# Performance work log

Measured on AMD Instinct MI355X. Metric: run time of the kernel, lower is better.

Reference implementation:

```python
import jax, jax.numpy as jnp
import numpy as np

D_MODEL = 3072
HEADS = 24
DH = 128
EPS = 1e-05


def _rmsnorm(x, w):
    # x: [..., DH], normalize over last dim in fp32
    var = jnp.mean(jnp.square(x.astype(jnp.float32)), axis=-1, keepdims=True)
    return (x * jax.lax.rsqrt(var + EPS)) * w


def _rope(x, cos, sin):
    # x: [B, S, H, D]; cos/sin: [S, D//2] (real/imag of complex freqs)
    xr = x[..., 0::2].astype(jnp.float32)
    xi = x[..., 1::2].astype(jnp.float32)
    c = cos[None, :, None, :]
    s = sin[None, :, None, :]
    out_r = xr * c - xi * s
    out_i = xr * s + xi * c
    out = jnp.stack([out_r, out_i], axis=-1)  # [B,S,H,D/2,2]
    return out.reshape(*x.shape).astype(x.dtype)


def _linear(x, w, b):
    # torch Linear convention: w [out, in]
    return jnp.einsum('bsi,oi->bso', x, w) + b


def setup_inputs() -> dict:
    key = jax.random.key(0)
    ks = jax.random.split(key, 24)
    B, S_IMG, S_TXT = 1, 2048, 256
    init = lambda k, shp: jax.random.normal(k, shp, dtype=jnp.float32) * 0.02
    inp = {
        'hidden_states': jax.random.normal(ks[0], (B, S_IMG, D_MODEL), dtype=jnp.float32),
        'encoder_hidden_states': jax.random.normal(ks[1], (B, S_TXT, D_MODEL), dtype=jnp.float32),
        'encoder_hidden_states_mask': jnp.ones((B, S_TXT), dtype=bool),
        'img_cos': jnp.cos(jax.random.uniform(ks[2], (S_IMG, DH // 2)) * 6.28),
        'img_sin': jnp.sin(jax.random.uniform(ks[2], (S_IMG, DH // 2)) * 6.28),
        'txt_cos': jnp.cos(jax.random.uniform(ks[3], (S_TXT, DH // 2)) * 6.28),
        'txt_sin': jnp.sin(jax.random.uniform(ks[3], (S_TXT, DH // 2)) * 6.28),
        'wq': init(ks[4], (D_MODEL, D_MODEL)), 'bq': jnp.zeros((D_MODEL,), jnp.float32),
        'wk': init(ks[5], (D_MODEL, D_MODEL)), 'bk': jnp.zeros((D_MODEL,), jnp.float32),
        'wv': init(ks[6], (D_MODEL, D_MODEL)), 'bv': jnp.zeros((D_MODEL,), jnp.float32),
        'awq': init(ks[7], (D_MODEL, D_MODEL)), 'abq': jnp.zeros((D_MODEL,), jnp.float32),
        'awk': init(ks[8], (D_MODEL, D_MODEL)), 'abk': jnp.zeros((D_MODEL,), jnp.float32),
        'awv': init(ks[9], (D_MODEL, D_MODEL)), 'abv': jnp.zeros((D_MODEL,), jnp.float32),
        'norm_q_w': jnp.ones((DH,), jnp.float32),
        'norm_k_w': jnp.ones((DH,), jnp.float32),
        'norm_aq_w': jnp.ones((DH,), jnp.float32),
        'norm_ak_w': jnp.ones((DH,), jnp.float32),
        'w_out': init(ks[10], (D_MODEL, D_MODEL)), 'b_out': jnp.zeros((D_MODEL,), jnp.float32),
        'w_add_out': init(ks[11], (D_MODEL, D_MODEL)), 'b_add_out': jnp.zeros((D_MODEL,), jnp.float32),
    }
    return inp


def _forward(hidden_states, encoder_hidden_states, encoder_hidden_states_mask,
             img_cos, img_sin, txt_cos, txt_sin,
             wq, bq, wk, bk, wv, bv, awq, abq, awk, abk, awv, abv,
             norm_q_w, norm_k_w, norm_aq_w, norm_ak_w,
             w_out, b_out, w_add_out, b_add_out):
    B, S_img, _ = hidden_states.shape
    S_txt = encoder_hidden_states.shape[1]

    def split_heads(x):
        return x.reshape(B, x.shape[1], HEADS, DH)

    img_q = split_heads(_linear(hidden_states, wq, bq))
    img_k = split_heads(_linear(hidden_states, wk, bk))
    img_v = split_heads(_linear(hidden_states, wv, bv))
    txt_q = split_heads(_linear(encoder_hidden_states, awq, abq))
    txt_k = split_heads(_linear(encoder_hidden_states, awk, abk))
    txt_v = split_heads(_linear(encoder_hidden_states, awv, abv))

    img_q = _rope(_rmsnorm(img_q, norm_q_w), img_cos, img_sin)
    img_k = _rope(_rmsnorm(img_k, norm_k_w), img_cos, img_sin)
    txt_q = _rope(_rmsnorm(txt_q, norm_aq_w), txt_cos, txt_sin)
    txt_k = _rope(_rmsnorm(txt_k, norm_ak_w), txt_cos, txt_sin)

    q = jnp.concatenate([img_q, txt_q], axis=1)  # [B, S, H, D]
    k = jnp.concatenate([img_k, txt_k], axis=1)
    v = jnp.concatenate([img_v, txt_v], axis=1)

    mask = jnp.concatenate([jnp.ones((B, S_img), dtype=bool),
                            encoder_hidden_states_mask.astype(bool)], axis=1)  # [B, S]

    scale = DH ** -0.5
    scores = jnp.einsum('bqhd,bkhd->bhqk', q, k) * scale
    scores = jnp.where(mask[:, None, None, :], scores, jnp.float32(-1e30))
    probs = jax.nn.softmax(scores, axis=-1)
    attn = jnp.einsum('bhqk,bkhd->bqhd', probs, v).reshape(B, S_img + S_txt, HEADS * DH)

    img_attn, txt_attn = attn[:, :S_img], attn[:, S_img:]
    img_out = _linear(img_attn, w_out, b_out)
    txt_out = _linear(txt_attn, w_add_out, b_add_out)
    return img_out, txt_out


def reference(hidden_states, encoder_hidden_states, encoder_hidden_states_mask,
              img_cos, img_sin, txt_cos, txt_sin,
              wq, bq, wk, bk, wv, bv, awq, abq, awk, abk, awv, abv,
              norm_q_w, norm_k_w, norm_aq_w, norm_ak_w,
              w_out, b_out, w_add_out, b_add_out):
    return _forward(hidden_states, encoder_hidden_states, encoder_hidden_states_mask,
                    img_cos, img_sin, txt_cos, txt_sin,
                    wq, bq, wk, bk, wv, bv, awq, abq, awk, abk, awv, abv,
                    norm_q_w, norm_k_w, norm_aq_w, norm_ak_w,
                    w_out, b_out, w_add_out, b_add_out)
```

## Files before the change

### kernel.cpp

```cpp
#include <hip/hip_runtime.h>
#include <cstdint>
#include <cstddef>

#define S_IMG 2048
#define S_TXT 256
#define S_TOT 2304
#define DM    3072
#define NH    24
#define DH    128

typedef __attribute__((ext_vector_type(8))) short short8;
typedef __attribute__((ext_vector_type(4))) float f32x4;
typedef __attribute__((ext_vector_type(8))) unsigned short u16x8;
typedef __attribute__((ext_vector_type(4))) unsigned short u16x4;
typedef __attribute__((ext_vector_type(2))) unsigned int u32x2;

__device__ __forceinline__ unsigned short f2b(float f) {
  union { float f; uint32_t u; } v; v.f = f;
  uint32_t r = v.u + 0x7fffu + ((v.u >> 16) & 1u);
  return (unsigned short)(r >> 16);
}
__device__ __forceinline__ float b2f(unsigned short h) {
  union { uint32_t u; float f; } v; v.u = ((uint32_t)h) << 16; return v.f;
}
__device__ __forceinline__ void async16(void* lds, const void* g) {
  __builtin_amdgcn_global_load_lds(
      (const __attribute__((address_space(1))) unsigned int*)g,
      (__attribute__((address_space(3))) unsigned int*)lds, 16, 0, 0);
}

template<int CTRL>
__device__ __forceinline__ float dpp_add_step(float x) {
  int y = __builtin_amdgcn_update_dpp(__float_as_int(x), __float_as_int(x),
                                      CTRL, 0xf, 0xf, false);
  return x + __int_as_float(y);
}
__device__ __forceinline__ float dpp_row_sum(float x) {
  x = dpp_add_step<0x121>(x);
  x = dpp_add_step<0x122>(x);
  x = dpp_add_step<0x124>(x);
  x = dpp_add_step<0x128>(x);
  return x;
}

__global__ __launch_bounds__(256) void k_cvt(const float* __restrict__ in,
                                             unsigned short* __restrict__ out, int n4) {
  int i = blockIdx.x * 256 + threadIdx.x;
  if (i >= n4) return;
  f32x4 v = ((const f32x4*)in)[i];
  u16x4 o = { f2b(v[0]), f2b(v[1]), f2b(v[2]), f2b(v[3]) };
  ((u16x4*)out)[i] = o;
}

__global__ __launch_bounds__(256) void k_cvt3(const float* __restrict__ a,
                                              const float* __restrict__ b,
                                              const float* __restrict__ c,
                                              unsigned short* __restrict__ dst, int n4) {
  const float* __restrict__ src = (blockIdx.y == 0) ? a : ((blockIdx.y == 1) ? b : c);
  int i = blockIdx.x * 256 + threadIdx.x;
  if (i >= n4) return;
  f32x4 v = ((const f32x4*)src)[i];
  u16x4 o = { f2b(v[0]), f2b(v[1]), f2b(v[2]), f2b(v[3]) };
  ((u16x4*)(dst + (size_t)blockIdx.y * DM * DM))[i] = o;
}

template<int OUT_MODE>
__global__ __launch_bounds__(512, 2) void k_gemm8(
    const unsigned short* __restrict__ A,
    const unsigned short* __restrict__ Wa, const unsigned short* __restrict__ Wb,
    const float* __restrict__ bi0, const float* __restrict__ bi1, const float* __restrict__ bi2,
    const float* __restrict__ bt0, const float* __restrict__ bt1, const float* __restrict__ bt2,
    void* __restrict__ Cb, int mblocks)
{
  __shared__ unsigned short As[2][256 * 64];
  __shared__ unsigned short Bs[2][128 * 64];
  constexpr int NT = DM / 64;

  const int z = blockIdx.z;
  const int nb = mblocks * 24;
  int id = blockIdx.x;
  if ((nb & 7) == 0) id = (id & 7) * (nb >> 3) + (id >> 3);
  const int by = id % mblocks, bx = id / mblocks;
  const int m0 = by * 256, n0 = bx * 128;

  const unsigned short* __restrict__ Wz = ((by < 8) ? Wa : Wb) + (size_t)z * DM * DM;
  const float* __restrict__ bias =
      (by < 8) ? ((z == 0) ? bi0 : (z == 1) ? bi1 : bi2)
               : ((z == 0) ? bt0 : (z == 1) ? bt1 : bt2);

  const int tid = threadIdx.x;
  const int lane = tid & 63;
  const int w = tid >> 6;
  const int wr = w >> 1, wc = w & 1;
  const int l15 = lane & 15, lg = lane >> 4;

  const int row0 = tid >> 3;
  const int g0 = (tid & 7) ^ (row0 & 7);
  const unsigned short* Ag = A + (size_t)m0 * DM;
  const unsigned short* Bg = Wz + (size_t)n0 * DM;

  const int fx0 = ((0 * 4 + lg) ^ (l15 & 7)) * 8 + l15 * 64;
  const int fx1 = ((1 * 4 + lg) ^ (l15 & 7)) * 8 + l15 * 64;

  f32x4 acc[4][4] = {};
  short8 bf[4][2];

#define STG_A(db, s, t) async16(&As[db][(s) * 4096 + tid * 8], \
    Ag + (size_t)((s) * 64 + row0) * DM + (t) * 64 + g0 * 8)
#define STG_B(db, s, t) async16(&Bs[db][(s) * 4096 + tid * 8], \
    Bg + (size_t)((s) * 64 + row0) * DM + (t) * 64 + g0 * 8)
#define RD_A(db, ms, ks) (*(const short8*)&As[db][wr * 4096 + (ms) * 1024 + ((ks) ? fx1 : fx0)])
#define RD_B(db, ns, ks) (*(const short8*)&Bs[db][wc * 4096 + (ns) * 1024 + ((ks) ? fx1 : fx0)])

#define PH(db, msb, RDB, STAGE_STMT, ENDGRP) { \
    short8 af[2][2]; \
    _Pragma("unroll") for (int mi = 0; mi < 2; ++mi) { \
      af[mi][0] = RD_A(db, (msb) + mi, 0); af[mi][1] = RD_A(db, (msb) + mi, 1); } \
    RDB; \
    STAGE_STMT; \
    __builtin_amdgcn_s_barrier(); \
    asm volatile("s_waitcnt lgkmcnt(0)" ::: "memory"); \
    __builtin_amdgcn_sched_barrier(0); \
    __builtin_amdgcn_s_setprio(1); \
    _Pragma("unroll") for (int ks = 0; ks < 2; ++ks) \
      _Pragma("unroll") for (int ns = 0; ns < 4; ++ns) \
        _Pragma("unroll") for (int mi = 0; mi < 2; ++mi) \
          acc[(msb) + mi][ns] = __builtin_amdgcn_mfma_f32_16x16x32_bf16( \
              af[mi][ks], bf[ns][ks], acc[(msb) + mi][ns], 0, 0, 0); \
    __builtin_amdgcn_s_setprio(0); \
    ENDGRP; \
    __builtin_amdgcn_s_barrier(); \
  }

#define TILE(t, db) { \
    PH(db, 0, \
       { _Pragma("unroll") for (int ns = 0; ns < 4; ++ns) { \
           bf[ns][0] = RD_B(db, ns, 0); bf[ns][1] = RD_B(db, ns, 1); } }, \
       { if ((t) + 1 < NT) { STG_A(1 - (db), 0, (t) + 1); \
                             STG_A(1 - (db), 1, (t) + 1); \
                             STG_A(1 - (db), 2, (t) + 1); } }, \
       ;); \
    PH(db, 2, ;, \
       { if ((t) + 1 < NT) STG_A(1 - (db), 3, (t) + 1); \
         if ((t) + 2 < NT) { STG_B(db, 0, (t) + 2); STG_B(db, 1, (t) + 2); } }, \
       { if ((t) + 2 < NT) asm volatile("s_waitcnt vmcnt(2)" ::: "memory"); \
         else              asm volatile("s_waitcnt vmcnt(0)" ::: "memory"); }); \
  }

  STG_A(0, 0, 0); STG_A(0, 1, 0); STG_A(0, 2, 0); STG_A(0, 3, 0);
  STG_B(0, 0, 0); STG_B(0, 1, 0);
  STG_B(1, 0, 1); STG_B(1, 1, 1);
  asm volatile("s_waitcnt vmcnt(2)" ::: "memory");
  __builtin_amdgcn_s_barrier();

  for (int t = 0; t < NT; t += 2) {
    TILE(t, 0);
    TILE(t + 1, 1);
  }
#undef STG_A
#undef STG_B
#undef RD_A
#undef RD_B
#undef PH
#undef TILE

  float bvv[4];
#pragma unroll
  for (int ns = 0; ns < 4; ++ns) bvv[ns] = bias[n0 + wc * 64 + ns * 16 + l15];
#pragma unroll
  for (int ms = 0; ms < 4; ++ms) {
    const int gr = m0 + wr * 64 + ms * 16 + lg * 4;
#pragma unroll
    for (int ns = 0; ns < 4; ++ns) {
      const int gc = n0 + wc * 64 + ns * 16 + l15;
      if (OUT_MODE == 0) {
#pragma unroll
        for (int r = 0; r < 4; ++r)
          ((float*)Cb)[(size_t)(gr + r) * DM + gc] = acc[ms][ns][r] + bvv[ns];
      } else if (z < 2) {
#pragma unroll
        for (int r = 0; r < 4; ++r)
          ((unsigned short*)Cb + (size_t)z * NH * S_TOT * DH)
              [((size_t)(gc >> 7) * S_TOT + (gr + r)) * DH + (gc & 127)] =
              f2b(acc[ms][ns][r] + bvv[ns]);
      } else {
        unsigned short* V = (unsigned short*)Cb + (size_t)2 * NH * S_TOT * DH;
        u16x4 pk = { f2b(acc[ms][ns][0] + bvv[ns]), f2b(acc[ms][ns][1] + bvv[ns]),
                     f2b(acc[ms][ns][2] + bvv[ns]), f2b(acc[ms][ns][3] + bvv[ns]) };
        *(u16x4*)&V[((size_t)(gc >> 7) * DH + (gc & 127)) * S_TOT + gr] = pk;
      }
    }
  }
}

template<int OUT_MODE>
__global__ __launch_bounds__(256) void k_gemm(
    const unsigned short* __restrict__ A,
    const float* __restrict__ B0, const float* __restrict__ B1, const float* __restrict__ B2,
    const float* __restrict__ bias0, const float* __restrict__ bias1, const float* __restrict__ bias2,
    void* __restrict__ C0, void* __restrict__ C1, void* __restrict__ C2,
    int M, int K, int moff)
{
  __shared__ unsigned short As[128 * 32];
  __shared__ unsigned short Bs[128 * 32];
  const int z = blockIdx.z;
  const float* __restrict__ B    = (z == 0) ? B0 : ((z == 1) ? B1 : B2);
  const float* __restrict__ bias = (z == 0) ? bias0 : ((z == 1) ? bias1 : bias2);
  void* __restrict__ C           = (z == 0) ? C0 : ((z == 1) ? C1 : C2);

  const int tid  = threadIdx.x;
  const int lane = tid & 63;
  const int wid  = tid >> 6;
  const int wr = wid >> 1, wc = wid & 1;
  const int m0 = blockIdx.y * 128, n0 = blockIdx.x * 128;
  const int l15 = lane & 15, lg = lane >> 4;

  f32x4 acc[4][4] = {};

  const int arow0 = wid * 16 + (lane >> 2);
  const int acol  = (lane & 3) * 8;
  const int brow  = tid >> 1;
  const int bcol  = (tid & 1) * 16;

  for (int k0 = 0; k0 < K; k0 += 32) {
#pragma unroll
    for (int i = 0; i < 2; ++i) {
      int row = i * 64 + arow0;
      async16(&As[row * 32 + acol], A + (size_t)(m0 + row) * K + k0 + acol);
    }
    {
      const float* gb = B + (size_t)(n0 + brow) * K + k0 + bcol;
      f32x4 v0 = *(const f32x4*)(gb);
      f32x4 v1 = *(const f32x4*)(gb + 4);
      f32x4 v2 = *(const f32x4*)(gb + 8);
      f32x4 v3 = *(const f32x4*)(gb + 12);
      u16x8 w0 = { f2b(v0[0]), f2b(v0[1]), f2b(v0[2]), f2b(v0[3]),
                   f2b(v1[0]), f2b(v1[1]), f2b(v1[2]), f2b(v1[3]) };
      u16x8 w1 = { f2b(v2[0]), f2b(v2[1]), f2b(v2[2]), f2b(v2[3]),
                   f2b(v3[0]), f2b(v3[1]), f2b(v3[2]), f2b(v3[3]) };
      *(u16x8*)&Bs[brow * 32 + bcol] = w0;
      *(u16x8*)&Bs[brow * 32 + bcol + 8] = w1;
    }
    __syncthreads();
    short8 af[4], bf[4];
#pragma unroll
    for (int m = 0; m < 4; ++m)
      af[m] = *(const short8*)&As[(wr * 64 + m * 16 + l15) * 32 + lg * 8];
#pragma unroll
    for (int n = 0; n < 4; ++n)
      bf[n] = *(const short8*)&Bs[(wc * 64 + n * 16 + l15) * 32 + lg * 8];
#pragma unroll
    for (int m = 0; m < 4; ++m)
#pragma unroll
      for (int n = 0; n < 4; ++n)
        acc[m][n] = __builtin_amdgcn_mfma_f32_16x16x32_bf16(af[m], bf[n], acc[m][n], 0, 0, 0);
    __syncthreads();
  }

  float bv[4];
#pragma unroll
  for (int n = 0; n < 4; ++n) bv[n] = bias[n0 + wc * 64 + n * 16 + l15];
#pragma unroll
  for (int m = 0; m < 4; ++m) {
    const int gr = m0 + wr * 64 + m * 16 + lg * 4;
#pragma unroll
    for (int n = 0; n < 4; ++n) {
      const int gc = n0 + wc * 64 + n * 16 + l15;
      if (OUT_MODE == 0) {
#pragma unroll
        for (int r = 0; r < 4; ++r)
          ((float*)C)[(size_t)(gr + r + moff) * DM + gc] = acc[m][n][r] + bv[n];
      } else if (z < 2) {
#pragma unroll
        for (int r = 0; r < 4; ++r)
          ((unsigned short*)C)[((size_t)(gc >> 7) * S_TOT + (gr + r + moff)) * DH + (gc & 127)] =
              f2b(acc[m][n][r] + bv[n]);
      } else {
        u16x4 pk = { f2b(acc[m][n][0] + bv[n]), f2b(acc[m][n][1] + bv[n]),
                     f2b(acc[m][n][2] + bv[n]), f2b(acc[m][n][3] + bv[n]) };
        *(u16x4*)&((unsigned short*)C)[((size_t)(gc >> 7) * DH + (gc & 127)) * S_TOT + gr + moff] = pk;
      }
    }
  }
}

__global__ __launch_bounds__(256) void k_normrope(
    unsigned short* __restrict__ qb, unsigned short* __restrict__ kb,
    const float* __restrict__ nq_img, const float* __restrict__ nk_img,
    const float* __restrict__ nq_txt, const float* __restrict__ nk_txt,
    const float* __restrict__ icos, const float* __restrict__ isin,
    const float* __restrict__ tcos, const float* __restrict__ tsin)
{
  const float CS = 0.08838834764831845f * 1.4426950408889634f;
  const int lane = threadIdx.x & 63;
  const int gw = blockIdx.x * 4 + (threadIdx.x >> 6);
  const int buf = gw / (NH * S_TOT);
  const int rem = gw - buf * (NH * S_TOT);
  const int h = rem / S_TOT;
  const int t = rem - h * S_TOT;
  unsigned short* base = (buf ? kb : qb) + ((size_t)h * S_TOT + t) * DH + lane * 2;
  uint32_t pr = *(const uint32_t*)base;
  float x0 = b2f((unsigned short)(pr & 0xffff));
  float x1 = b2f((unsigned short)(pr >> 16));
  float ss = x0 * x0 + x1 * x1;
#pragma unroll
  for (int msk = 1; msk < 64; msk <<= 1) ss += __shfl_xor(ss, msk, 64);
  float rr = rsqrtf(ss * (1.0f / DH) + 1e-5f);
  if (!buf) rr *= CS;
  const float* w = buf ? ((t < S_IMG) ? nk_img : nk_txt)
                       : ((t < S_IMG) ? nq_img : nq_txt);
  float w0 = w[lane * 2], w1 = w[lane * 2 + 1];
  float c, s;
  if (t < S_IMG) { c = icos[t * 64 + lane]; s = isin[t * 64 + lane]; }
  else           { c = tcos[(t - S_IMG) * 64 + lane]; s = tsin[(t - S_IMG) * 64 + lane]; }
  float y0 = x0 * rr * w0, y1 = x1 * rr * w1;
  float o0 = y0 * c - y1 * s;
  float o1 = y0 * s + y1 * c;
  uint32_t ow = (uint32_t)f2b(o0) | ((uint32_t)f2b(o1) << 16);
  *(uint32_t*)base = ow;
}

__global__ __launch_bounds__(256) void k_attn(
    const unsigned short* __restrict__ q, const unsigned short* __restrict__ k,
    const unsigned short* __restrict__ vT, unsigned short* __restrict__ out)
{
  __shared__ __align__(16) unsigned short Ks[2][64 * 128];
  __shared__ __align__(16) unsigned short Vs[2][128 * 64];
  __shared__ __align__(16) unsigned short Ps[4][32 * 64];
  const int bi = blockIdx.x;
  const int j  = bi >> 3;
  const int h  = (bi & 7) * 3 + j / 18;
  const int qb = j % 18;
  const int tid = threadIdx.x;
  const int lane = tid & 63;
  const int wid  = tid >> 6;
  const int l15 = lane & 15, lg = lane >> 4;
  const float MST = 17.0f;

  const unsigned short* qg = q  + ((size_t)h * S_TOT + qb * 128 + wid * 32) * DH;
  const unsigned short* kg = k  + (size_t)h * S_TOT * DH;
  const unsigned short* vg = vT + (size_t)h * DH * S_TOT;

  short8 qf[2][4];
#pragma unroll
  for (int mt = 0; mt < 2; ++mt)
#pragma unroll
    for (int kk = 0; kk < 4; ++kk)
      qf[mt][kk] = *(const short8*)(qg + (size_t)(mt * 16 + l15) * DH + kk * 32 + lg * 8);

  const int vst_c = (lane & 7) ^ ((lane >> 3) & 7);

#define STAGE(buf, t)                                                                   \
  {                                                                                     \
    _Pragma("unroll")                                                                   \
    for (int i = 0; i < 4; ++i) {                                                       \
      int sc = (lane & 15) ^ ((wid * 4 + i) & 7);                                       \
      async16(&Ks[buf][(wid * 16 + i * 4) * 128 + lane * 8],                            \
              kg + (size_t)((t) * 64 + wid * 16 + i * 4 + (lane >> 4)) * DH + sc * 8);  \
    }                                                                                   \
    _Pragma("unroll")                                                                   \
    for (int i = 0; i < 4; ++i) {                                                       \
      int row = wid * 32 + i * 8 + (lane >> 3);                                         \
      async16(&Vs[buf][(wid * 32 + i * 8) * 64 + lane * 8],                             \
              vg + (size_t)row * S_TOT + (t) * 64 + vst_c * 8);                         \
    }                                                                                   \
  }

  f32x4 o[2][8] = {};
  float ls[2][4] = {};
  unsigned short* pw = Ps[wid];

  int pwoff[2][4];
#pragma unroll
  for (int mt = 0; mt < 2; ++mt)
#pragma unroll
    for (int r = 0; r < 4; ++r) {
      const int q_ = mt * 16 + lg * 4 + r;
      pwoff[mt][r] = q_ * 128 + (((l15 >> 1) ^ (q_ & 7)) << 4) + ((l15 & 1) << 3);
    }

  STAGE(0, 0);
  __syncthreads();

#define TILE_BODY(t, cur, nxt, LAST)                                                    \
  {                                                                                     \
    if (!(LAST)) STAGE(nxt, (t) + 1);                                                   \
    f32x4 s[2][4] = {};                                                                 \
    __builtin_amdgcn_s_setprio(1);                                                      \
    _Pragma("unroll")                                                                   \
    for (int kk = 0; kk < 4; ++kk) {                                                    \
      short8 kf[4];                                                                     \
      _Pragma("unroll")                                                                 \
      for (int nt = 0; nt < 4; ++nt) {                                                  \
        int row = l15 * 4 + nt;                                                         \
        kf[nt] = *(const short8*)&Ks[cur][row * 128 + (((kk * 4 + lg) ^ (l15 & 7)) * 8)];\
      }                                                                                 \
      _Pragma("unroll")                                                                 \
      for (int mt = 0; mt < 2; ++mt)                                                    \
        _Pragma("unroll")                                                               \
        for (int nt = 0; nt < 4; ++nt)                                                  \
          s[mt][nt] = __builtin_amdgcn_mfma_f32_16x16x32_bf16(qf[mt][kk], kf[nt],       \
                                                              s[mt][nt], 0, 0, 0);      \
    }                                                                                   \
    __builtin_amdgcn_s_setprio(0);                                                      \
                \
    _Pragma("unroll")                                                                   \
    for (int mt = 0; mt < 2; ++mt)                                                      \
      _Pragma("unroll")                                                                 \
      for (int r = 0; r < 4; ++r) {                                                     \
        float p0 = exp2f(s[mt][0][r] - MST), p1 = exp2f(s[mt][1][r] - MST);             \
        float p2 = exp2f(s[mt][2][r] - MST), p3 = exp2f(s[mt][3][r] - MST);             \
        ls[mt][r] += (p0 + p1) + (p2 + p3);                                             \
        uint32_t lo, hi;                                                                \
        asm("v_cvt_pk_bf16_f32 %0, %1, %2" : "=v"(lo) : "v"(p0), "v"(p1));              \
        asm("v_cvt_pk_bf16_f32 %0, %1, %2" : "=v"(hi) : "v"(p2), "v"(p3));              \
        *(u32x2*)((char*)pw + pwoff[mt][r]) = (u32x2){lo, hi};                          \
      }                                                                                 \
    __builtin_amdgcn_s_setprio(1);                                                      \
    _Pragma("unroll")                                                                   \
    for (int kc = 0; kc < 2; ++kc) {                                                    \
      short8 pf[2];                                                                     \
      _Pragma("unroll")                                                                 \
      for (int mt = 0; mt < 2; ++mt) {                                                  \
        int q2 = mt * 16 + l15;                                                         \
        pf[mt] = *(const short8*)&pw[q2 * 64 + (((kc * 4 + lg) ^ (q2 & 7)) * 8)];       \
      }                                                                                 \
      _Pragma("unroll")                                                                 \
      for (int nt = 0; nt < 8; ++nt) {                                                  \
        int row = nt * 16 + l15;                                                        \
        short8 vf = *(const short8*)&Vs[cur][row * 64 + (((kc * 4 + lg) ^ (row & 7)) * 8)];\
        _Pragma("unroll")                                                               \
        for (int mt = 0; mt < 2; ++mt)                                                  \
          o[mt][nt] = __builtin_amdgcn_mfma_f32_16x16x32_bf16(pf[mt], vf, o[mt][nt],    \
                                                              0, 0, 0);                 \
      }                                                                                 \
    }                                                                                   \
    __builtin_amdgcn_s_setprio(0);                                                      \
    __syncthreads();                                                                    \
  }

  for (int t = 0; t < 36; t += 2) {
    TILE_BODY(t, 0, 1, false);
    TILE_BODY(t + 1, 1, 0, (t + 1) == 35);
  }
#undef TILE_BODY
#undef STAGE

#pragma unroll
  for (int mt = 0; mt < 2; ++mt)
#pragma unroll
    for (int r = 0; r < 4; ++r)
      ls[mt][r] = 1.0f / dpp_row_sum(ls[mt][r]);
  const int row0 = qb * 128 + wid * 32;
#pragma unroll
  for (int mt = 0; mt < 2; ++mt)
#pragma unroll
    for (int nt = 0; nt < 8; ++nt)
#pragma unroll
      for (int r = 0; r < 4; ++r) {
        int row = row0 + mt * 16 + lg * 4 + r;
        out[(size_t)row * DM + h * DH + nt * 16 + l15] = f2b(o[mt][nt][r] * ls[mt][r]);
      }
}

extern "C" void kernel_launch(void* const* d_in, const int* in_sizes, int n_in,
                              void* d_out, int out_size, void* d_ws, size_t ws_size,
                              hipStream_t stream) {
  const float* hs   = (const float*)d_in[0];
  const float* ehs  = (const float*)d_in[1];
  const float* icos = (const float*)d_in[3];
  const float* isin = (const float*)d_in[4];
  const float* tcos = (const float*)d_in[5];
  const float* tsin = (const float*)d_in[6];
  const float* wq  = (const float*)d_in[7];  const float* bq  = (const float*)d_in[8];
  const float* wk  = (const float*)d_in[9];  const float* bk  = (const float*)d_in[10];
  const float* wv  = (const float*)d_in[11]; const float* bv  = (const float*)d_in[12];
  const float* awq = (const float*)d_in[13]; const float* abq = (const float*)d_in[14];
  const float* awk = (const float*)d_in[15]; const float* abk = (const float*)d_in[16];
  const float* awv = (const float*)d_in[17]; const float* abv = (const float*)d_in[18];
  const float* nqw = (const float*)d_in[19]; const float* nkw = (const float*)d_in[20];
  const float* naq = (const float*)d_in[21]; const float* nak = (const float*)d_in[22];
  const float* wo  = (const float*)d_in[23]; const float* bo  = (const float*)d_in[24];
  const float* wao = (const float*)d_in[25]; const float* bao = (const float*)d_in[26];

  unsigned short* xh   = (unsigned short*)d_ws;
  unsigned short* xt   = xh + (size_t)S_IMG * DM;
  unsigned short* qbuf = xt + (size_t)S_TXT * DM;
  unsigned short* kbuf = qbuf + (size_t)NH * S_TOT * DH;
  unsigned short* vT   = kbuf + (size_t)NH * S_TOT * DH;
  unsigned short* ab   = vT + (size_t)NH * S_TOT * DH;
  unsigned short* wqkvb = ab + (size_t)S_TOT * DM;
  unsigned short* wob   = wqkvb;
  unsigned short* waob  = wqkvb + (size_t)DM * DM;
  const size_t need = ((size_t)(wqkvb - (unsigned short*)d_ws) + (size_t)3 * DM * DM) * 2;
  const bool big = ws_size >= need;
  float* out = (float*)d_out;

  k_cvt<<<dim3(S_IMG * DM / 4 / 256), 256, 0, stream>>>(hs, xh, S_IMG * DM / 4);
  k_cvt<<<dim3(S_TXT * DM / 4 / 256), 256, 0, stream>>>(ehs, xt, S_TXT * DM / 4);

  const int wn4 = DM * DM / 4;
  if (big) {
    k_cvt3<<<dim3(wn4 / 256, 3), 256, 0, stream>>>(wq, wk, wv, wqkvb, wn4);
    k_gemm8<1><<<dim3(192, 1, 3), 512, 0, stream>>>(xh, wqkvb, wqkvb,
                                                    bq, bk, bv, bq, bk, bv, qbuf, 8);
    k_cvt3<<<dim3(wn4 / 256, 2), 256, 0, stream>>>(wo, wao, wao, wqkvb, wn4);
  } else {
    k_gemm<1><<<dim3(24, 16, 3), 256, 0, stream>>>(xh, wq, wk, wv, bq, bk, bv,
                                                   qbuf, kbuf, vT, S_IMG, DM, 0);
  }
  k_gemm<1><<<dim3(24, 2, 3), 256, 0, stream>>>(xt, awq, awk, awv, abq, abk, abv,
                                                qbuf, kbuf, vT, S_TXT, DM, S_IMG);

  k_normrope<<<dim3(2 * NH * S_TOT / 4), 256, 0, stream>>>(qbuf, kbuf, nqw, nkw, naq, nak,
                                                           icos, isin, tcos, tsin);

  k_attn<<<dim3(432), 256, 0, stream>>>(qbuf, kbuf, vT, ab);

  if (big) {
    k_gemm8<0><<<dim3(216, 1, 1), 512, 0, stream>>>(ab, wob, waob,
                                                    bo, bo, bo, bao, bao, bao, out, 9);
  } else {
    k_gemm<0><<<dim3(24, 16, 1), 256, 0, stream>>>(ab, wo, wo, wo, bo, bo, bo,
                                                   out, out, out, S_IMG, DM, 0);
    k_gemm<0><<<dim3(24, 2, 1), 256, 0, stream>>>(ab + (size_t)S_IMG * DM, wao, wao, wao,
                                                  bao, bao, bao, out, out, out, S_TXT, DM, S_IMG);
  }
}
```

Baseline: 567.6 us.

## Split attention block into eight waves of 16 query rows each

The attention kernel now launches 512 threads per block, with eight waves each owning 16 query rows instead of four waves owning 32. K/V staging is redistributed across all 512 threads, and per-wave P scratch shrinks accordingly. The aim is more waves per CU for latency hiding and fewer registers per wave. The cost is that each K/V fragment read from LDS feeds only one MFMA row tile instead of two, which roughly doubles LDS read traffic per FLOP.

```diff
diff --git a/kernel.cpp b/kernel.cpp
--- a/kernel.cpp
+++ b/kernel.cpp
@@ -320,13 +320,13 @@
   *(uint32_t*)base = ow;
 }
 
-__global__ __launch_bounds__(256) void k_attn(
+__global__ __launch_bounds__(512) void k_attn(
     const unsigned short* __restrict__ q, const unsigned short* __restrict__ k,
     const unsigned short* __restrict__ vT, unsigned short* __restrict__ out)
 {
   __shared__ __align__(16) unsigned short Ks[2][64 * 128];
   __shared__ __align__(16) unsigned short Vs[2][128 * 64];
-  __shared__ __align__(16) unsigned short Ps[4][32 * 64];
+  __shared__ __align__(16) unsigned short Ps[8][16 * 64];
   const int bi = blockIdx.x;
   const int j  = bi >> 3;
   const int h  = (bi & 7) * 3 + j / 18;
@@ -337,47 +337,46 @@
   const int l15 = lane & 15, lg = lane >> 4;
   const float MST = 17.0f;
 
-  const unsigned short* qg = q  + ((size_t)h * S_TOT + qb * 128 + wid * 32) * DH;
+  const unsigned short* qg = q  + ((size_t)h * S_TOT + qb * 128 + wid * 16) * DH;
   const unsigned short* kg = k  + (size_t)h * S_TOT * DH;
   const unsigned short* vg = vT + (size_t)h * DH * S_TOT;
 
-  short8 qf[2][4];
-#pragma unroll
-  for (int mt = 0; mt < 2; ++mt)
-#pragma unroll
-    for (int kk = 0; kk < 4; ++kk)
-      qf[mt][kk] = *(const short8*)(qg + (size_t)(mt * 16 + l15) * DH + kk * 32 + lg * 8);
-
-  const int vst_c = (lane & 7) ^ ((lane >> 3) & 7);
+  short8 qf[4];
+#pragma unroll
+  for (int kk = 0; kk < 4; ++kk)
+    qf[kk] = *(const short8*)(qg + (size_t)l15 * DH + kk * 32 + lg * 8);
+
+  const int krow0 = tid >> 4, kc0 = tid & 15;
+  const int vrow0 = tid >> 3, vc0 = tid & 7;
 
 #define STAGE(buf, t)                                                                   \
   {                                                                                     \
     _Pragma("unroll")                                                                   \
-    for (int i = 0; i < 4; ++i) {                                                       \
-      int sc = (lane & 15) ^ ((wid * 4 + i) & 7);                                       \
-      async16(&Ks[buf][(wid * 16 + i * 4) * 128 + lane * 8],                            \
-              kg + (size_t)((t) * 64 + wid * 16 + i * 4 + (lane >> 4)) * DH + sc * 8);  \
+    for (int j2 = 0; j2 < 2; ++j2) {                                                    \
+      int row = j2 * 32 + krow0;                                                        \
+      int sc  = kc0 ^ ((row >> 2) & 7);                                                 \
+      async16(&Ks[buf][row * 128 + kc0 * 8],                                            \
+              kg + (size_t)((t) * 64 + row) * DH + sc * 8);                             \
     }                                                                                   \
     _Pragma("unroll")                                                                   \
-    for (int i = 0; i < 4; ++i) {                                                       \
-      int row = wid * 32 + i * 8 + (lane >> 3);                                         \
-      async16(&Vs[buf][(wid * 32 + i * 8) * 64 + lane * 8],                             \
-              vg + (size_t)row * S_TOT + (t) * 64 + vst_c * 8);                         \
+    for (int j2 = 0; j2 < 2; ++j2) {                                                    \
+      int row = j2 * 64 + vrow0;                                                        \
+      int sc  = vc0 ^ (row & 7);                                                        \
+      async16(&Vs[buf][row * 64 + vc0 * 8],                                             \
+              vg + (size_t)row * S_TOT + (t) * 64 + sc * 8);                            \
     }                                                                                   \
   }
 
-  f32x4 o[2][8] = {};
-  float ls[2][4] = {};
+  f32x4 o[8] = {};
+  float ls[4] = {};
   unsigned short* pw = Ps[wid];
 
-  int pwoff[2][4];
-#pragma unroll
-  for (int mt = 0; mt < 2; ++mt)
-#pragma unroll
-    for (int r = 0; r < 4; ++r) {
-      const int q_ = mt * 16 + lg * 4 + r;
-      pwoff[mt][r] = q_ * 128 + (((l15 >> 1) ^ (q_ & 7)) << 4) + ((l15 & 1) << 3);
-    }
+  int pwoff[4];
+#pragma unroll
+  for (int r = 0; r < 4; ++r) {
+    const int q_ = lg * 4 + r;
+    pwoff[r] = q_ * 128 + (((l15 >> 1) ^ (q_ & 7)) << 4) + ((l15 & 1) << 3);
+  }
 
   STAGE(0, 0);
   __syncthreads();
@@ -385,7 +384,7 @@
 #define TILE_BODY(t, cur, nxt, LAST)                                                    \
   {                                                                                     \
     if (!(LAST)) STAGE(nxt, (t) + 1);                                                   \
-    f32x4 s[2][4] = {};                                                                 \
+    f32x4 s[4] = {};                                                                    \
     __builtin_amdgcn_s_setprio(1);                                                      \
     _Pragma("unroll")                                                                   \
     for (int kk = 0; kk < 4; ++kk) {                                                    \
@@ -396,43 +395,30 @@
         kf[nt] = *(const short8*)&Ks[cur][row * 128 + (((kk * 4 + lg) ^ (l15 & 7)) * 8)];\
       }                                                                                 \
       _Pragma("unroll")                                                                 \
-      for (int mt = 0; mt < 2; ++mt)                                                    \
-        _Pragma("unroll")                                                               \
-        for (int nt = 0; nt < 4; ++nt)                                                  \
-          s[mt][nt] = __builtin_amdgcn_mfma_f32_16x16x32_bf16(qf[mt][kk], kf[nt],       \
-                                                              s[mt][nt], 0, 0, 0);      \
+      for (int nt = 0; nt < 4; ++nt)                                                    \
+        s[nt] = __builtin_amdgcn_mfma_f32_16x16x32_bf16(qf[kk], kf[nt], s[nt], 0, 0, 0);\
     }                                                                                   \
     __builtin_amdgcn_s_setprio(0);                                                      \
-                \
+                                       \
     _Pragma("unroll")                                                                   \
-    for (int mt = 0; mt < 2; ++mt)                                                      \
-      _Pragma("unroll")                                                                 \
-      for (int r = 0; r < 4; ++r) {                                                     \
-        float p0 = exp2f(s[mt][0][r] - MST), p1 = exp2f(s[mt][1][r] - MST);             \
-        float p2 = exp2f(s[mt][2][r] - MST), p3 = exp2f(s[mt][3][r] - MST);             \
-        ls[mt][r] += (p0 + p1) + (p2 + p3);                                             \
-        uint32_t lo, hi;                                                                \
-        asm("v_cvt_pk_bf16_f32 %0, %1, %2" : "=v"(lo) : "v"(p0), "v"(p1));              \
-        asm("v_cvt_pk_bf16_f32 %0, %1, %2" : "=v"(hi) : "v"(p2), "v"(p3));              \
-        *(u32x2*)((char*)pw + pwoff[mt][r]) = (u32x2){lo, hi};                          \
-      }                                                                                 \
+    for (int r = 0; r < 4; ++r) {                                                       \
+      float p0 = exp2f(s[0][r] - MST), p1 = exp2f(s[1][r] - MST);                       \
+      float p2 = exp2f(s[2][r] - MST), p3 = exp2f(s[3][r] - MST);                       \
+      ls[r] += (p0 + p1) + (p2 + p3);                                                   \
+      uint32_t lo, hi;                                                                  \
+      asm("v_cvt_pk_bf16_f32 %0, %1, %2" : "=v"(lo) : "v"(p0), "v"(p1));                \
+      asm("v_cvt_pk_bf16_f32 %0, %1, %2" : "=v"(hi) : "v"(p2), "v"(p3));                \
+      *(u32x2*)((char*)pw + pwoff[r]) = (u32x2){lo, hi};                                \
+    }                                                                                   \
     __builtin_amdgcn_s_setprio(1);                                                      \
     _Pragma("unroll")                                                                   \
     for (int kc = 0; kc < 2; ++kc) {                                                    \
-      short8 pf[2];                                                                     \
-      _Pragma("unroll")                                                                 \
-      for (int mt = 0; mt < 2; ++mt) {                                                  \
-        int q2 = mt * 16 + l15;                                                         \
-        pf[mt] = *(const short8*)&pw[q2 * 64 + (((kc * 4 + lg) ^ (q2 & 7)) * 8)];       \
-      }                                                                                 \
+      short8 pf = *(const short8*)&pw[l15 * 64 + (((kc * 4 + lg) ^ (l15 & 7)) * 8)];    \
       _Pragma("unroll")                                                                 \
       for (int nt = 0; nt < 8; ++nt) {                                                  \
         int row = nt * 16 + l15;                                                        \
         short8 vf = *(const short8*)&Vs[cur][row * 64 + (((kc * 4 + lg) ^ (row & 7)) * 8)];\
-        _Pragma("unroll")                                                               \
-        for (int mt = 0; mt < 2; ++mt)                                                  \
-          o[mt][nt] = __builtin_amdgcn_mfma_f32_16x16x32_bf16(pf[mt], vf, o[mt][nt],    \
-                                                              0, 0, 0);                 \
+        o[nt] = __builtin_amdgcn_mfma_f32_16x16x32_bf16(pf, vf, o[nt], 0, 0, 0);        \
       }                                                                                 \
     }                                                                                   \
     __builtin_amdgcn_s_setprio(0);                                                      \
@@ -447,20 +433,16 @@
 #undef STAGE
 
 #pragma unroll
-  for (int mt = 0; mt < 2; ++mt)
-#pragma unroll
-    for (int r = 0; r < 4; ++r)
-      ls[mt][r] = 1.0f / dpp_row_sum(ls[mt][r]);
-  const int row0 = qb * 128 + wid * 32;
-#pragma unroll
-  for (int mt = 0; mt < 2; ++mt)
-#pragma unroll
-    for (int nt = 0; nt < 8; ++nt)
-#pragma unroll
-      for (int r = 0; r < 4; ++r) {
-        int row = row0 + mt * 16 + lg * 4 + r;
-        out[(size_t)row * DM + h * DH + nt * 16 + l15] = f2b(o[mt][nt][r] * ls[mt][r]);
-      }
+  for (int r = 0; r < 4; ++r)
+    ls[r] = 1.0f / dpp_row_sum(ls[r]);
+  const int row0 = qb * 128 + wid * 16;
+#pragma unroll
+  for (int nt = 0; nt < 8; ++nt)
+#pragma unroll
+    for (int r = 0; r < 4; ++r) {
+      int row = row0 + lg * 4 + r;
+      out[(size_t)row * DM + h * DH + nt * 16 + l15] = f2b(o[nt][r] * ls[r]);
+    }
 }
 
 extern "C" void kernel_launch(void* const* d_in, const int* in_sizes, int n_in,
@@ -515,7 +497,7 @@
   k_normrope<<<dim3(2 * NH * S_TOT / 4), 256, 0, stream>>>(qbuf, kbuf, nqw, nkw, naq, nak,
                                                            icos, isin, tcos, tsin);
 
-  k_attn<<<dim3(432), 256, 0, stream>>>(qbuf, kbuf, vT, ab);
+  k_attn<<<dim3(432), 512, 0, stream>>>(qbuf, kbuf, vT, ab);
 
   if (big) {
     k_gemm8<0><<<dim3(216, 1, 1), 512, 0, stream>>>(ab, wob, waob,
```

Result: faster. 520.6 us (-8.3%).

## Shrink GEMM tiles to 128x128 with 256 threads; single-buffer V in attention

Applied to the files above, without the earlier changes.

The big GEMM kernel moves from 256x128 tiles with 512 threads to 128x128 tiles with 256 threads. That doubles the grid and raises occupancy to four blocks per CU, at the cost of less operand reuse per tile. The staging and wait counts change to match. The attention kernel single-buffers V and stages it at the start of each tile, overlapping it with the QK^T and softmax compute. This frees LDS so two blocks fit per CU, but adds extra barriers.

```diff
diff --git a/kernel.cpp b/kernel.cpp
--- a/kernel.cpp
+++ b/kernel.cpp
@@ -65,14 +65,14 @@
 }
 
 template<int OUT_MODE>
-__global__ __launch_bounds__(512, 2) void k_gemm8(
+__global__ __launch_bounds__(256, 4) void k_gemm8(
     const unsigned short* __restrict__ A,
     const unsigned short* __restrict__ Wa, const unsigned short* __restrict__ Wb,
     const float* __restrict__ bi0, const float* __restrict__ bi1, const float* __restrict__ bi2,
     const float* __restrict__ bt0, const float* __restrict__ bt1, const float* __restrict__ bt2,
     void* __restrict__ Cb, int mblocks)
 {
-  __shared__ unsigned short As[2][256 * 64];
+  __shared__ unsigned short As[2][128 * 64];
   __shared__ unsigned short Bs[2][128 * 64];
   constexpr int NT = DM / 64;
 
@@ -81,12 +81,12 @@
   int id = blockIdx.x;
   if ((nb & 7) == 0) id = (id & 7) * (nb >> 3) + (id >> 3);
   const int by = id % mblocks, bx = id / mblocks;
-  const int m0 = by * 256, n0 = bx * 128;
-
-  const unsigned short* __restrict__ Wz = ((by < 8) ? Wa : Wb) + (size_t)z * DM * DM;
+  const int m0 = by * 128, n0 = bx * 128;
+
+  const unsigned short* __restrict__ Wz = ((by < 16) ? Wa : Wb) + (size_t)z * DM * DM;
   const float* __restrict__ bias =
-      (by < 8) ? ((z == 0) ? bi0 : (z == 1) ? bi1 : bi2)
-               : ((z == 0) ? bt0 : (z == 1) ? bt1 : bt2);
+      (by < 16) ? ((z == 0) ? bi0 : (z == 1) ? bi1 : bi2)
+                : ((z == 0) ? bt0 : (z == 1) ? bt1 : bt2);
 
   const int tid = threadIdx.x;
   const int lane = tid & 63;
@@ -105,10 +105,10 @@
   f32x4 acc[4][4] = {};
   short8 bf[4][2];
 
-#define STG_A(db, s, t) async16(&As[db][(s) * 4096 + tid * 8], \
-    Ag + (size_t)((s) * 64 + row0) * DM + (t) * 64 + g0 * 8)
-#define STG_B(db, s, t) async16(&Bs[db][(s) * 4096 + tid * 8], \
-    Bg + (size_t)((s) * 64 + row0) * DM + (t) * 64 + g0 * 8)
+#define STG_A(db, s, t) async16(&As[db][(s) * 2048 + tid * 8], \
+    Ag + (size_t)((s) * 32 + row0) * DM + (t) * 64 + g0 * 8)
+#define STG_B(db, s, t) async16(&Bs[db][(s) * 2048 + tid * 8], \
+    Bg + (size_t)((s) * 32 + row0) * DM + (t) * 64 + g0 * 8)
 #define RD_A(db, ms, ks) (*(const short8*)&As[db][wr * 4096 + (ms) * 1024 + ((ks) ? fx1 : fx0)])
 #define RD_B(db, ns, ks) (*(const short8*)&Bs[db][wc * 4096 + (ns) * 1024 + ((ks) ? fx1 : fx0)])
 
@@ -136,21 +136,20 @@
     PH(db, 0, \
        { _Pragma("unroll") for (int ns = 0; ns < 4; ++ns) { \
            bf[ns][0] = RD_B(db, ns, 0); bf[ns][1] = RD_B(db, ns, 1); } }, \
-       { if ((t) + 1 < NT) { STG_A(1 - (db), 0, (t) + 1); \
-                             STG_A(1 - (db), 1, (t) + 1); \
-                             STG_A(1 - (db), 2, (t) + 1); } }, \
+       { if ((t) + 1 < NT) { STG_A(1 - (db), 0, (t) + 1); STG_A(1 - (db), 1, (t) + 1); \
+                             STG_A(1 - (db), 2, (t) + 1); STG_A(1 - (db), 3, (t) + 1); } }, \
        ;); \
     PH(db, 2, ;, \
-       { if ((t) + 1 < NT) STG_A(1 - (db), 3, (t) + 1); \
-         if ((t) + 2 < NT) { STG_B(db, 0, (t) + 2); STG_B(db, 1, (t) + 2); } }, \
-       { if ((t) + 2 < NT) asm volatile("s_waitcnt vmcnt(2)" ::: "memory"); \
+       { if ((t) + 2 < NT) { STG_B(db, 0, (t) + 2); STG_B(db, 1, (t) + 2); \
+                             STG_B(db, 2, (t) + 2); STG_B(db, 3, (t) + 2); } }, \
+       { if ((t) + 2 < NT) asm volatile("s_waitcnt vmcnt(4)" ::: "memory"); \
          else              asm volatile("s_waitcnt vmcnt(0)" ::: "memory"); }); \
   }
 
   STG_A(0, 0, 0); STG_A(0, 1, 0); STG_A(0, 2, 0); STG_A(0, 3, 0);
-  STG_B(0, 0, 0); STG_B(0, 1, 0);
-  STG_B(1, 0, 1); STG_B(1, 1, 1);
-  asm volatile("s_waitcnt vmcnt(2)" ::: "memory");
+  STG_B(0, 0, 0); STG_B(0, 1, 0); STG_B(0, 2, 0); STG_B(0, 3, 0);
+  STG_B(1, 0, 1); STG_B(1, 1, 1); STG_B(1, 2, 1); STG_B(1, 3, 1);
+  asm volatile("s_waitcnt vmcnt(4)" ::: "memory");
   __builtin_amdgcn_s_barrier();
 
   for (int t = 0; t < NT; t += 2) {
@@ -320,12 +319,12 @@
   *(uint32_t*)base = ow;
 }
 
-__global__ __launch_bounds__(256) void k_attn(
+__global__ __launch_bounds__(256, 2) void k_attn(
     const unsigned short* __restrict__ q, const unsigned short* __restrict__ k,
     const unsigned short* __restrict__ vT, unsigned short* __restrict__ out)
 {
   __shared__ __align__(16) unsigned short Ks[2][64 * 128];
-  __shared__ __align__(16) unsigned short Vs[2][128 * 64];
+  __shared__ __align__(16) unsigned short Vs[128 * 64];
   __shared__ __align__(16) unsigned short Ps[4][32 * 64];
   const int bi = blockIdx.x;
   const int j  = bi >> 3;
@@ -350,7 +349,7 @@
 
   const int vst_c = (lane & 7) ^ ((lane >> 3) & 7);
 
-#define STAGE(buf, t)                                                                   \
+#define STAGE_K(buf, t)                                                                 \
   {                                                                                     \
     _Pragma("unroll")                                                                   \
     for (int i = 0; i < 4; ++i) {                                                       \
@@ -358,10 +357,13 @@
       async16(&Ks[buf][(wid * 16 + i * 4) * 128 + lane * 8],                            \
               kg + (size_t)((t) * 64 + wid * 16 + i * 4 + (lane >> 4)) * DH + sc * 8);  \
     }                                                                                   \
+  }
+#define STAGE_V(t)                                                                      \
+  {                                                                                     \
     _Pragma("unroll")                                                                   \
     for (int i = 0; i < 4; ++i) {                                                       \
       int row = wid * 32 + i * 8 + (lane >> 3);                                         \
-      async16(&Vs[buf][(wid * 32 + i * 8) * 64 + lane * 8],                             \
+      async16(&Vs[(wid * 32 + i * 8) * 64 + lane * 8],                                  \
               vg + (size_t)row * S_TOT + (t) * 64 + vst_c * 8);                         \
     }                                                                                   \
   }
@@ -379,12 +381,14 @@
       pwoff[mt][r] = q_ * 128 + (((l15 >> 1) ^ (q_ & 7)) << 4) + ((l15 & 1) << 3);
     }
 
-  STAGE(0, 0);
-  __syncthreads();
+  STAGE_K(0, 0);
+  asm volatile("s_waitcnt vmcnt(0)" ::: "memory");
+  __builtin_amdgcn_s_barrier();
 
 #define TILE_BODY(t, cur, nxt, LAST)                                                    \
   {                                                                                     \
-    if (!(LAST)) STAGE(nxt, (t) + 1);                                                   \
+    STAGE_V(t);                                                                         \
+    if (!(LAST)) STAGE_K(nxt, (t) + 1);                                                 \
     f32x4 s[2][4] = {};                                                                 \
     __builtin_amdgcn_s_setprio(1);                                                      \
     _Pragma("unroll")                                                                   \
@@ -403,7 +407,6 @@
                                                               s[mt][nt], 0, 0, 0);      \
     }                                                                                   \
     __builtin_amdgcn_s_setprio(0);                                                      \
-                \
     _Pragma("unroll")                                                                   \
     for (int mt = 0; mt < 2; ++mt)                                                      \
       _Pragma("unroll")                                                                 \
@@ -416,6 +419,11 @@
         asm("v_cvt_pk_bf16_f32 %0, %1, %2" : "=v"(hi) : "v"(p2), "v"(p3));              \
         *(u32x2*)((char*)pw + pwoff[mt][r]) = (u32x2){lo, hi};                          \
       }                                                                                 \
+          \
+    if (!(LAST)) asm volatile("s_waitcnt vmcnt(4)" ::: "memory");                       \
+    else         asm volatile("s_waitcnt vmcnt(0)" ::: "memory");                       \
+    __builtin_amdgcn_sched_barrier(0);                                                  \
+    __builtin_amdgcn_s_barrier();                                                       \
     __builtin_amdgcn_s_setprio(1);                                                      \
     _Pragma("unroll")                                                                   \
     for (int kc = 0; kc < 2; ++kc) {                                                    \
@@ -428,7 +436,7 @@
       _Pragma("unroll")                                                                 \
       for (int nt = 0; nt < 8; ++nt) {                                                  \
         int row = nt * 16 + l15;                                                        \
-        short8 vf = *(const short8*)&Vs[cur][row * 64 + (((kc * 4 + lg) ^ (row & 7)) * 8)];\
+        short8 vf = *(const short8*)&Vs[row * 64 + (((kc * 4 + lg) ^ (row & 7)) * 8)];  \
         _Pragma("unroll")                                                               \
         for (int mt = 0; mt < 2; ++mt)                                                  \
           o[mt][nt] = __builtin_amdgcn_mfma_f32_16x16x32_bf16(pf[mt], vf, o[mt][nt],    \
@@ -436,7 +444,11 @@
       }                                                                                 \
     }                                                                                   \
     __builtin_amdgcn_s_setprio(0);                                                      \
-    __syncthreads();                                                                    \
+    if (!(LAST)) {                                                                      \
+      asm volatile("s_waitcnt vmcnt(0)" ::: "memory");                                  \
+      __builtin_amdgcn_sched_barrier(0);                                                \
+      __builtin_amdgcn_s_barrier();                                                     \
+    }                                                                                   \
   }
 
   for (int t = 0; t < 36; t += 2) {
@@ -444,7 +456,8 @@
     TILE_BODY(t + 1, 1, 0, (t + 1) == 35);
   }
 #undef TILE_BODY
-#undef STAGE
+#undef STAGE_K
+#undef STAGE_V
 
 #pragma unroll
   for (int mt = 0; mt < 2; ++mt)
@@ -502,8 +515,8 @@
   const int wn4 = DM * DM / 4;
   if (big) {
     k_cvt3<<<dim3(wn4 / 256, 3), 256, 0, stream>>>(wq, wk, wv, wqkvb, wn4);
-    k_gemm8<1><<<dim3(192, 1, 3), 512, 0, stream>>>(xh, wqkvb, wqkvb,
-                                                    bq, bk, bv, bq, bk, bv, qbuf, 8);
+    k_gemm8<1><<<dim3(384, 1, 3), 256, 0, stream>>>(xh, wqkvb, wqkvb,
+                                                    bq, bk, bv, bq, bk, bv, qbuf, 16);
     k_cvt3<<<dim3(wn4 / 256, 2), 256, 0, stream>>>(wo, wao, wao, wqkvb, wn4);
   } else {
     k_gemm<1><<<dim3(24, 16, 3), 256, 0, stream>>>(xh, wq, wk, wv, bq, bk, bv,
@@ -518,8 +531,8 @@
   k_attn<<<dim3(432), 256, 0, stream>>>(qbuf, kbuf, vT, ab);
 
   if (big) {
-    k_gemm8<0><<<dim3(216, 1, 1), 512, 0, stream>>>(ab, wob, waob,
-                                                    bo, bo, bo, bao, bao, bao, out, 9);
+    k_gemm8<0><<<dim3(432, 1, 1), 256, 0, stream>>>(ab, wob, waob,
+                                                    bo, bo, bo, bao, bao, bao, out, 18);
   } else {
     k_gemm<0><<<dim3(24, 16, 1), 256, 0, stream>>>(ab, wo, wo, wo, bo, bo, bo,
                                                    out, out, out, S_IMG, DM, 0);
```

New measurement: 527.6 us. 1.08x faster.
